# Optimization experiments

Hardware: AMD Instinct MI355X
Metric: run time of the kernel (lower is better)

Reference implementation:

```python
import jax, jax.numpy as jnp
import numpy as np

NUM_HEADS = 12
NUM_PATCHES = 196


def _make_relative_distance_index(num_patches=NUM_PATCHES):
    size = int(np.sqrt(num_patches))  # 14
    coords = np.stack(np.meshgrid(np.arange(size), np.arange(size), indexing='ij'))  # [2,14,14]
    flat = coords.reshape(2, -1)  # [2,196]
    rel = flat[:, None, :] - flat[:, :, None]  # [2,196,196]
    rel = rel.transpose(1, 2, 0).astype(np.int64)  # [196,196,2]
    rel[:, :, 0] += size - 1
    rel[:, :, 1] += size - 1
    rel[:, :, 0] *= 2 * size - 1
    idx = rel.sum(-1) + 1  # shift for cls slot at table row 0
    full = np.zeros((num_patches + 1, num_patches + 1), dtype=np.int64)
    full[1:, 1:] = idx
    return full


def setup_inputs() -> dict:
    key = jax.random.key(0)
    k1, k2, k3, k4, k5 = jax.random.split(key, 5)
    B, N, C = 64, NUM_PATCHES + 1, 768
    table_size = (2 * int(np.sqrt(NUM_PATCHES)) - 1) ** 2 + 1  # 730
    x = jax.random.normal(k1, (B, N, C), dtype=jnp.float32)
    table = jax.random.normal(k2, (table_size, NUM_HEADS), dtype=jnp.float32) * 0.02
    w_qkv = jax.random.normal(k3, (3 * C, C), dtype=jnp.float32) * 0.02
    w_proj = jax.random.normal(k4, (C, C), dtype=jnp.float32) * 0.02
    b_proj = jax.random.normal(k5, (C,), dtype=jnp.float32) * 0.02
    rel_index = jnp.asarray(_make_relative_distance_index())
    return {"x": x, "table": table, "w_qkv": w_qkv, "w_proj": w_proj,
            "b_proj": b_proj, "rel_index": rel_index}


def reference(x, table, w_qkv, w_proj, b_proj, rel_index):
    B, N, C = x.shape
    H = NUM_HEADS
    hd = C // H
    scale = hd ** -0.5
    # qkv projection: [B,N,3C] -> [3,B,H,N,hd]
    qkv = (x @ w_qkv.T).reshape(B, N, 3, H, hd).transpose(2, 0, 3, 1, 4)
    q, k, v = qkv[0], qkv[1], qkv[2]
    # gathered relative position bias: [N,N,H] -> [H,N,N]
    bias = table[rel_index].transpose(2, 0, 1)
    scores = jnp.einsum('bhnd,bhmd->bhnm', q, k) * scale + bias[None]
    attn = jax.nn.softmax(scores, axis=-1)
    out = jnp.einsum('bhnm,bhmd->bhnd', attn, v)
    out = out.transpose(0, 2, 1, 3).reshape(B, N, C)
    return out @ w_proj.T + b_proj
```

## Files before the change

### kernel.cpp

```cpp
#include <hip/hip_runtime.h>


#define NB   64
#define NN   197
#define NC   768
#define NH   12
#define HD   64
#define MM   (NB*NN)
#define MR   12672
#define NP   208
#define PS   208
#define VTS  216
#define SZQ  ((size_t)NB * NH * NN * HD)
#define CVTQ ((MM + 2304 + 768) * 192)
#define BIASN (NH * 13 * 13 * 256)

typedef unsigned short ushort_t;
typedef __attribute__((ext_vector_type(8))) short short8;
typedef __attribute__((ext_vector_type(4))) float f32x4;
union U128 { uint4 u; short8 s; };

__device__ __forceinline__ unsigned bf16_rne(float f) {
    unsigned u = __float_as_uint(f);
    return (u + 0x7fffu + ((u >> 16) & 1u)) >> 16;
}

__device__ __forceinline__ void gld16(unsigned short* lds, const unsigned short* g) {
    __builtin_amdgcn_global_load_lds(
        (const __attribute__((address_space(1))) void*)g,
        (__attribute__((address_space(3))) void*)lds, 16, 0, 0);
}

__global__ __launch_bounds__(256) void prepare(
    const float* __restrict__ x, const float* __restrict__ w_qkv,
    const float* __restrict__ w_proj, const float* __restrict__ table,
    const int* __restrict__ rel_index,
    ushort_t* __restrict__ xh, ushort_t* __restrict__ wh,
    ushort_t* __restrict__ wp, float* __restrict__ biasP)
{
    int idx = blockIdx.x * 256 + threadIdx.x;
    if (idx < CVTQ) {
        int r = idx / 192;
        int c = (idx - r * 192) * 4;
        const float* src;
        ushort_t* dsth;
        if (r < MM) {
            src = x + (size_t)r * NC; dsth = xh + (size_t)r * NC + c;
        } else if (r < MM + 2304) {
            int rr = r - MM;
            src = w_qkv + (size_t)rr * NC; dsth = wh + (size_t)rr * NC + c;
        } else {
            int rr = r - MM - 2304;
            src = w_proj + (size_t)rr * NC; dsth = wp + (size_t)rr * NC + c;
        }
        float4 f = *(const float4*)(src + c);
        ushort4 hv = { (ushort_t)bf16_rne(f.x), (ushort_t)bf16_rne(f.y),
                       (ushort_t)bf16_rne(f.z), (ushort_t)bf16_rne(f.w) };
        *(ushort4*)dsth = hv;
    } else {
        int i = idx - CVTQ;
        if (i < BIASN) {
            int r = i & 3, l15 = (i >> 2) & 15, quad = (i >> 6) & 3;
            int t = i >> 8;
            int kt = t % 13; int t2 = t / 13;
            int qt = t2 % 13; int h = t2 / 13;
            int n = qt * 16 + quad * 4 + r;
            int m = kt * 16 + l15;
            float v = -1e30f;
            if (n < NN && m < NN) v = table[rel_index[n * NN + m] * NH + h];
            biasP[i] = v;
        }
    }
}

__device__ __forceinline__ void gemm_mainloop(
    const ushort_t* __restrict__ A2, int sA,
    const ushort_t* __restrict__ B2, int sB,
    int m0, int n0, int kiters, ushort_t* Abuf, ushort_t* Bbuf, f32x4 acc[4][4])
{
    const int tid = threadIdx.x;
    const int w = tid >> 6, lane = tid & 63;
    const int wm = w & 1, wn = w >> 1;
    const int lr = lane >> 3, lc = lane & 7;
    const int gch = lc ^ lr;

    const ushort_t* Ag = A2 + (size_t)(m0 + w * 32 + lr) * sA + gch * 8;
    const ushort_t* Bg = B2 + (size_t)(n0 + w * 32 + lr) * sB + gch * 8;
    ushort_t* Al = Abuf + (w * 32) * 64;
    ushort_t* Bl = Bbuf + (w * 32) * 64;

    int aoff[4], boff[4];
    const int quad = lane >> 4, l15 = lane & 15;
    #pragma unroll
    for (int t = 0; t < 4; t++) {
        int ra = wm * 64 + t * 16 + l15;
        aoff[t] = ra * 64 + ((quad ^ (ra & 7)) << 3);
        int rb = wn * 64 + t * 16 + l15;
        boff[t] = rb * 64 + ((quad ^ (rb & 7)) << 3);
    }

    for (int ks = 0; ks < kiters; ks++) {
        __syncthreads();
        #pragma unroll
        for (int it = 0; it < 4; it++) {
            gld16(Al + it * 8 * 64, Ag + (size_t)it * 8 * sA);
            gld16(Bl + it * 8 * 64, Bg + (size_t)it * 8 * sB);
        }
        __syncthreads();
        #pragma unroll
        for (int k0 = 0; k0 < 2; k0++) {
            U128 af[4], bf[4];
            #pragma unroll
            for (int t = 0; t < 4; t++) {
                af[t].u = *(const uint4*)&Abuf[aoff[t] ^ (k0 << 5)];
                bf[t].u = *(const uint4*)&Bbuf[boff[t] ^ (k0 << 5)];
            }
            #pragma unroll
            for (int i = 0; i < 4; i++)
                #pragma unroll
                for (int j = 0; j < 4; j++)
                    acc[i][j] = __builtin_amdgcn_mfma_f32_16x16x32_bf16(
                        af[i].s, bf[j].s, acc[i][j], 0, 0, 0);
        }
        Ag += 64; Bg += 64;
    }
}

__device__ __forceinline__ int xcd_remap(int bid, int nwg) {
    int q8 = nwg >> 3, r8 = nwg & 7;
    int xcd = bid & 7, loc = bid >> 3;
    return (xcd < r8 ? xcd * (q8 + 1) : r8 * (q8 + 1) + (xcd - r8) * q8) + loc;
}

__global__ __launch_bounds__(256) void gemm_qkv_mfma(
    const ushort_t* __restrict__ A2, const ushort_t* __restrict__ B2,
    ushort_t* __restrict__ qbf, ushort_t* __restrict__ kbf,
    ushort_t* __restrict__ vbf)
{
    __shared__ ushort_t Abuf[128 * 64];
    __shared__ ushort_t Bbuf[128 * 64];
    f32x4 acc[4][4];
    f32x4 z = {0.f, 0.f, 0.f, 0.f};
    #pragma unroll
    for (int i = 0; i < 4; i++)
        #pragma unroll
        for (int j = 0; j < 4; j++) acc[i][j] = z;

    int f = xcd_remap(blockIdx.x, 1782);
    int mt_ = f / 18, nt_ = f - mt_ * 18;
    const int m0 = mt_ * 128, n0 = nt_ * 128;
    gemm_mainloop(A2, NC, B2, NC, m0, n0, 12, Abuf, Bbuf, acc);

    __syncthreads();

    const int tid = threadIdx.x;
    const int w = tid >> 6, lane = tid & 63;
    const int wm = w & 1, wn = w >> 1;
    const int quad = lane >> 4, l15 = lane & 15;

    int c0b = n0 + wn * 64;
    int tq = c0b / NC;
    int wi = c0b - tq * NC;
    int hh = wi >> 6;
    ushort_t* dst = (tq == 0) ? qbf : (tq == 1) ? kbf : vbf;
    float scale = (tq == 0) ? 0.125f : 1.0f;

    ushort_t* Sw = Abuf + w * 1152;
    const int orow = lane >> 2;
    const int dch = (lane & 3) << 3;
    #pragma unroll
    for (int mt = 0; mt < 4; mt++) {
        #pragma unroll
        for (int nt = 0; nt < 4; nt++)
            #pragma unroll
            for (int r = 0; r < 4; r++)
                Sw[(quad * 4 + r) * 72 + nt * 16 + l15] =
                    (ushort_t)bf16_rne(acc[mt][nt][r] * scale);
        int m = m0 + wm * 64 + mt * 16 + orow;
        if (m < MM) {
            int b_ = m / NN, n_ = m - b_ * NN;
            size_t rb = ((size_t)(b_ * NH + hh) * NN + n_) * HD;
            uint4 v0 = *(const uint4*)&Sw[orow * 72 + dch];
            uint4 v1 = *(const uint4*)&Sw[orow * 72 + dch + 32];
            *(uint4*)&dst[rb + dch] = v0;
            *(uint4*)&dst[rb + dch + 32] = v1;
        }
    }
}

__global__ __launch_bounds__(256) void gemm_proj_mfma(
    const ushort_t* __restrict__ A2, const ushort_t* __restrict__ B2,
    const float* __restrict__ bias, float* __restrict__ out)
{
    __shared__ ushort_t Abuf[128 * 64];
    __shared__ ushort_t Bbuf[128 * 64];
    f32x4 acc[4][4];
    f32x4 z = {0.f, 0.f, 0.f, 0.f};
    #pragma unroll
    for (int i = 0; i < 4; i++)
        #pragma unroll
        for (int j = 0; j < 4; j++) acc[i][j] = z;

    int f = xcd_remap(blockIdx.x, 594);
    int mt_ = f / 6, nt_ = f - mt_ * 6;
    const int m0 = mt_ * 128, n0 = nt_ * 128;
    gemm_mainloop(A2, NC, B2, NC, m0, n0, 12, Abuf, Bbuf, acc);

    const int tid = threadIdx.x;
    const int w = tid >> 6, lane = tid & 63;
    const int wm = w & 1, wn = w >> 1;
    const int quad = lane >> 4, l15 = lane & 15;
    #pragma unroll
    for (int nt = 0; nt < 4; nt++) {
        int col = n0 + wn * 64 + nt * 16 + l15;
        float bi = bias[col];
        #pragma unroll
        for (int mt = 0; mt < 4; mt++) {
            #pragma unroll
            for (int r = 0; r < 4; r++) {
                int m = m0 + wm * 64 + mt * 16 + quad * 4 + r;
                if (m < MM)
                    out[(size_t)m * NC + col] = acc[mt][nt][r] + bi;
            }
        }
    }
}

__global__ __launch_bounds__(256, 3) void attn_mfma(
    const ushort_t* __restrict__ qbf, const ushort_t* __restrict__ kbf,
    const ushort_t* __restrict__ vbf, const float* __restrict__ biasP,
    ushort_t* __restrict__ ab)
{
    __shared__ ushort_t Vt[64 * VTS];
    __shared__ ushort_t Pl[4][16 * PS];

    const int bh = blockIdx.x;
    const int b = bh / NH, h = bh % NH;
    const int tid = threadIdx.x;
    const int w = tid >> 6, lane = tid & 63;
    const int quad = lane >> 4, l15 = lane & 15;
    const size_t base = (size_t)bh * (NN * HD);
    const ushort_t* kg = kbf + base;
    const ushort_t* vg = vbf + base;
    const ushort_t* qg = qbf + base;

    ushort_t* Vstage = &Pl[0][0];
    for (int idx = tid; idx < NP * 8; idx += 256) {
        int row = idx >> 3, ch = idx & 7;
        uint4 val = {0u, 0u, 0u, 0u};
        if (row < NN) val = *(const uint4*)(vg + (size_t)row * HD + ch * 8);
        *(uint4*)&Vstage[row * HD + ch * 8] = val;
    }
    __syncthreads();
    for (int task = tid; task < 64 * 26; task += 256) {
        int d = task & 63, kc = task >> 6;
        ushort_t tmp[8];
        #pragma unroll
        for (int j = 0; j < 8; j++)
            tmp[j] = Vstage[(kc * 8 + j) * HD + d];
        uint4 u;
        u.x = (unsigned)tmp[0] | ((unsigned)tmp[1] << 16);
        u.y = (unsigned)tmp[2] | ((unsigned)tmp[3] << 16);
        u.z = (unsigned)tmp[4] | ((unsigned)tmp[5] << 16);
        u.w = (unsigned)tmp[6] | ((unsigned)tmp[7] << 16);
        *(uint4*)&Vt[d * VTS + kc * 8] = u;
    }
    __syncthreads();

    #pragma unroll
    for (int rep = 0; rep < 4; rep++) {
        int qt = w + rep * 4;
        if (qt > 12) break;
        const int q0 = qt * 16;

        int qrow = q0 + l15; if (qrow > NN - 1) qrow = NN - 1;
        U128 qf0, qf1;
        qf0.u = *(const uint4*)(qg + (size_t)qrow * HD + quad * 8);
        qf1.u = *(const uint4*)(qg + (size_t)qrow * HD + 32 + quad * 8);

        f32x4 S[13];
        const float* bp = biasP + ((size_t)(h * 13 + qt) * 13) * 256 + (quad << 6) + (l15 << 2);
        #pragma unroll
        for (int kt = 0; kt < 13; kt++) {
            float4 bv = *(const float4*)(bp + kt * 256);
            S[kt][0] = bv.x; S[kt][1] = bv.y; S[kt][2] = bv.z; S[kt][3] = bv.w;
        }

        {
            U128 kf[13];
            #pragma unroll
            for (int kt = 0; kt < 13; kt++) {
                int krow = kt * 16 + l15; if (krow > NN - 1) krow = NN - 1;
                kf[kt].u = *(const uint4*)(kg + (size_t)krow * HD + quad * 8);
            }
            #pragma unroll
            for (int kt = 0; kt < 13; kt++)
                S[kt] = __builtin_amdgcn_mfma_f32_16x16x32_bf16(qf0.s, kf[kt].s, S[kt], 0, 0, 0);
            #pragma unroll
            for (int kt = 0; kt < 13; kt++) {
                int krow = kt * 16 + l15; if (krow > NN - 1) krow = NN - 1;
                kf[kt].u = *(const uint4*)(kg + (size_t)krow * HD + 32 + quad * 8);
            }
            #pragma unroll
            for (int kt = 0; kt < 13; kt++)
                S[kt] = __builtin_amdgcn_mfma_f32_16x16x32_bf16(qf1.s, kf[kt].s, S[kt], 0, 0, 0);
        }

        ushort_t* P = Pl[w];
        #pragma unroll
        for (int r = 0; r < 4; r++) {
            float mx = S[0][r];
            #pragma unroll
            for (int kt = 1; kt < 13; kt++) mx = fmaxf(mx, S[kt][r]);
            mx = fmaxf(mx, __shfl_xor(mx, 1));
            mx = fmaxf(mx, __shfl_xor(mx, 2));
            mx = fmaxf(mx, __shfl_xor(mx, 4));
            mx = fmaxf(mx, __shfl_xor(mx, 8));
            float sum = 0.f;
            #pragma unroll
            for (int kt = 0; kt < 13; kt++) {
                float e = __expf(S[kt][r] - mx);
                S[kt][r] = e;
                sum += e;
            }
            sum += __shfl_xor(sum, 1);
            sum += __shfl_xor(sum, 2);
            sum += __shfl_xor(sum, 4);
            sum += __shfl_xor(sum, 8);
            float inv = 1.0f / sum;
            int prow = quad * 4 + r;
            #pragma unroll
            for (int kt = 0; kt < 13; kt++)
                P[prow * PS + kt * 16 + l15] = (ushort_t)bf16_rne(S[kt][r] * inv);
        }

        f32x4 O[4];
        f32x4 z4 = {0.f, 0.f, 0.f, 0.f};
        #pragma unroll
        for (int dt = 0; dt < 4; dt++) O[dt] = z4;
        #pragma unroll
        for (int ks = 0; ks < 7; ks++) {
            int pc = ks * 32 + quad * 8;
            bool vld = (pc < NP);
            int pcc = vld ? pc : 0;
            U128 pf;
            pf.u = *(const uint4*)&P[l15 * PS + pcc];
            if (!vld) { pf.u.x = 0u; pf.u.y = 0u; pf.u.z = 0u; pf.u.w = 0u; }
            #pragma unroll
            for (int dt = 0; dt < 4; dt++) {
                U128 vf;
                vf.u = *(const uint4*)&Vt[(dt * 16 + l15) * VTS + pcc];
                O[dt] = __builtin_amdgcn_mfma_f32_16x16x32_bf16(pf.s, vf.s, O[dt], 0, 0, 0);
            }
        }

        float* Osh = (float*)&Pl[w][0];
        #pragma unroll
        for (int dt = 0; dt < 4; dt++)
            #pragma unroll
            for (int r = 0; r < 4; r++)
                Osh[(quad * 4 + r) * 68 + dt * 16 + l15] = O[dt][r];
        int orow = lane >> 2;
        int d0 = (lane & 3) << 4;
        int q = q0 + orow;
        if (q < NN) {
            unsigned hiw[8];
            #pragma unroll
            for (int k4 = 0; k4 < 4; k4++) {
                float4 f = *(const float4*)&Osh[orow * 68 + d0 + k4 * 4];
                unsigned h0 = bf16_rne(f.x), h1 = bf16_rne(f.y);
                unsigned h2 = bf16_rne(f.z), h3 = bf16_rne(f.w);
                hiw[k4 * 2]     = h0 | (h1 << 16);
                hiw[k4 * 2 + 1] = h2 | (h3 << 16);
            }
            size_t baseo = ((size_t)b * NN + q) * NC + h * HD + d0;
            uint4 hA = {hiw[0], hiw[1], hiw[2], hiw[3]};
            uint4 hB = {hiw[4], hiw[5], hiw[6], hiw[7]};
            *(uint4*)&ab[baseo] = hA;
            *(uint4*)&ab[baseo + 8] = hB;
        }
    }
}

extern "C" void kernel_launch(void* const* d_in, const int* in_sizes, int n_in,
                              void* d_out, int out_size, void* d_ws, size_t ws_size,
                              hipStream_t stream)
{
    const float* x        = (const float*)d_in[0];
    const float* table    = (const float*)d_in[1];
    const float* w_qkv    = (const float*)d_in[2];
    const float* w_proj   = (const float*)d_in[3];
    const float* b_proj   = (const float*)d_in[4];
    const int*   rel_idx  = (const int*)d_in[5];
    float* out = (float*)d_out;

    ushort_t* xh  = (ushort_t*)d_ws;
    ushort_t* wh  = xh + (size_t)MR * NC;
    ushort_t* wp  = wh + (size_t)2304 * NC;
    ushort_t* ab  = wp + (size_t)768 * NC;
    ushort_t* qbf = ab + (size_t)MR * NC;
    ushort_t* kbf = qbf + SZQ;
    ushort_t* vbf = kbf + SZQ;
    float* biasP  = (float*)(vbf + SZQ);

    const int ptot = CVTQ + BIASN;
    prepare<<<(ptot + 255) / 256, 256, 0, stream>>>(
        x, w_qkv, w_proj, table, rel_idx, xh, wh, wp, biasP);

    gemm_qkv_mfma<<<1782, 256, 0, stream>>>(xh, wh, qbf, kbf, vbf);
    attn_mfma<<<768, 256, 0, stream>>>(qbf, kbf, vbf, biasP, ab);
    gemm_proj_mfma<<<594, 256, 0, stream>>>(ab, wp, b_proj, out);
}
```

Before: 279.9 us.

## Stage K tile in XOR-swizzled LDS and read K fragments from shared memory

The attention kernel now loads the whole K tile for a head into LDS once, using an XOR swizzle on 16-byte chunks to avoid bank conflicts. QK^T fragments are then read from LDS instead of being fetched from global memory by every wave for every query tile. The V-transpose stride drops its padding (216 to 208), and the min-blocks-per-CU hint of 3 is removed. LDS use per block rises by about 26 KB, which may lower occupancy, and dropping the padding on Vt may bring back bank conflicts on the PV reads.

```diff
diff --git a/kernel.cpp b/kernel.cpp
--- a/kernel.cpp
+++ b/kernel.cpp
@@ -10,7 +10,6 @@
 #define MR   12672
 #define NP   208
 #define PS   208
-#define VTS  216
 #define SZQ  ((size_t)NB * NH * NN * HD)
 #define CVTQ ((MM + 2304 + 768) * 192)
 #define BIASN (NH * 13 * 13 * 256)
@@ -226,12 +225,13 @@
     }
 }
 
-__global__ __launch_bounds__(256, 3) void attn_mfma(
+__global__ __launch_bounds__(256) void attn_mfma(
     const ushort_t* __restrict__ qbf, const ushort_t* __restrict__ kbf,
     const ushort_t* __restrict__ vbf, const float* __restrict__ biasP,
     ushort_t* __restrict__ ab)
 {
-    __shared__ ushort_t Vt[64 * VTS];
+    __shared__ ushort_t Kl[NP * 64];
+    __shared__ ushort_t Vt[64 * PS];
     __shared__ ushort_t Pl[4][16 * PS];
 
     const int bh = blockIdx.x;
@@ -244,6 +244,13 @@
     const ushort_t* vg = vbf + base;
     const ushort_t* qg = qbf + base;
 
+    for (int idx = tid; idx < NP * 8; idx += 256) {
+        int row = idx >> 3, ch = idx & 7;
+        int srow = (row < NN) ? row : (NN - 1);
+        uint4 val = *(const uint4*)(kg + (size_t)srow * HD + ch * 8);
+        *(uint4*)&Kl[row * 64 + ((ch ^ (row & 7)) << 3)] = val;
+    }
+
     ushort_t* Vstage = &Pl[0][0];
     for (int idx = tid; idx < NP * 8; idx += 256) {
         int row = idx >> 3, ch = idx & 7;
@@ -263,9 +270,11 @@
         u.y = (unsigned)tmp[2] | ((unsigned)tmp[3] << 16);
         u.z = (unsigned)tmp[4] | ((unsigned)tmp[5] << 16);
         u.w = (unsigned)tmp[6] | ((unsigned)tmp[7] << 16);
-        *(uint4*)&Vt[d * VTS + kc * 8] = u;
+        *(uint4*)&Vt[d * PS + kc * 8] = u;
     }
     __syncthreads();
+
+    const int ksl = (quad ^ (l15 & 7)) << 3;
 
     #pragma unroll
     for (int rep = 0; rep < 4; rep++) {
@@ -286,24 +295,14 @@
             S[kt][0] = bv.x; S[kt][1] = bv.y; S[kt][2] = bv.z; S[kt][3] = bv.w;
         }
 
-        {
-            U128 kf[13];
-            #pragma unroll
-            for (int kt = 0; kt < 13; kt++) {
-                int krow = kt * 16 + l15; if (krow > NN - 1) krow = NN - 1;
-                kf[kt].u = *(const uint4*)(kg + (size_t)krow * HD + quad * 8);
-            }
-            #pragma unroll
-            for (int kt = 0; kt < 13; kt++)
-                S[kt] = __builtin_amdgcn_mfma_f32_16x16x32_bf16(qf0.s, kf[kt].s, S[kt], 0, 0, 0);
-            #pragma unroll
-            for (int kt = 0; kt < 13; kt++) {
-                int krow = kt * 16 + l15; if (krow > NN - 1) krow = NN - 1;
-                kf[kt].u = *(const uint4*)(kg + (size_t)krow * HD + 32 + quad * 8);
-            }
-            #pragma unroll
-            for (int kt = 0; kt < 13; kt++)
-                S[kt] = __builtin_amdgcn_mfma_f32_16x16x32_bf16(qf1.s, kf[kt].s, S[kt], 0, 0, 0);
+        #pragma unroll
+        for (int kt = 0; kt < 13; kt++) {
+            int ro = (kt * 16 + l15) * 64 + ksl;
+            U128 k0, k1;
+            k0.u = *(const uint4*)&Kl[ro];
+            k1.u = *(const uint4*)&Kl[ro ^ 32];
+            S[kt] = __builtin_amdgcn_mfma_f32_16x16x32_bf16(qf0.s, k0.s, S[kt], 0, 0, 0);
+            S[kt] = __builtin_amdgcn_mfma_f32_16x16x32_bf16(qf1.s, k1.s, S[kt], 0, 0, 0);
         }
 
         ushort_t* P = Pl[w];
@@ -349,7 +348,7 @@
             #pragma unroll
             for (int dt = 0; dt < 4; dt++) {
                 U128 vf;
-                vf.u = *(const uint4*)&Vt[(dt * 16 + l15) * VTS + pcc];
+                vf.u = *(const uint4*)&Vt[(dt * 16 + l15) * PS + pcc];
                 O[dt] = __builtin_amdgcn_mfma_f32_16x16x32_bf16(pf.s, vf.s, O[dt], 0, 0, 0);
             }
         }
```

New measurement: 249.9 us. -10.7%, faster.
